# Kernel optimization log

Hardware: AMD Instinct MI355X
Metric: run time of the kernel (lower is better)

The kernel has to match this reference:

```python
import jax, jax.numpy as jnp
import numpy as np

VOCAB, EMBED, HIDDEN, NCLS, PAD = 50257, 512, 1024, 4, 0

def setup_inputs() -> dict:
    key = jax.random.key(0)
    k1, k2, k3, k4, k5, k6 = jax.random.split(key, 6)
    emb = jax.random.uniform(k1, (VOCAB, EMBED), jnp.float32, -0.1, 0.1)
    emb = emb.at[PAD].set(0.0)
    W = jax.random.normal(k2, (HIDDEN, EMBED), jnp.float32) * (2.0 / (EMBED + HIDDEN)) ** 0.5
    b_w = jnp.zeros((HIDDEN,), jnp.float32)
    U = jax.random.normal(k3, (HIDDEN, HIDDEN), jnp.float32) * (1.0 / HIDDEN) ** 0.5
    V = jax.random.normal(k4, (NCLS, HIDDEN), jnp.float32) * (2.0 / (HIDDEN + NCLS)) ** 0.5
    b_v = jnp.zeros((NCLS,), jnp.float32)
    x = jax.random.randint(k5, (64, 512), 0, VOCAB, jnp.int32)
    return {"x": x, "emb": emb, "W": W, "b_w": b_w, "U": U, "V": V, "b_v": b_v}

def reference(x, emb, W, b_w, U, V, b_v):
    # x: [B, S] int tokens. Dropouts are identity (eval mode).
    embedded = emb[x]                      # [B, S, E]
    # Precompute Wx for all timesteps in one GEMM: [B, S, H]
    wx = jnp.einsum('bse,he->bsh', embedded, W) + b_w
    B = x.shape[0]
    h0 = jnp.zeros((B, W.shape[0]), embedded.dtype)

    def step(h, wx_t):
        h = jnp.tanh(wx_t + h @ U.T)       # [B, H]
        return h, None

    h_final, _ = jax.lax.scan(step, h0, jnp.swapaxes(wx, 0, 1))  # scan over S
    return h_final @ V.T + b_v             # [B, NCLS]
```

## Files before the change

kernel.cpp:

```cpp
#include <hip/hip_runtime.h>
#include <stdint.h>

#define B 64
#define S 512
#define E 512
#define H 1024
#define NCLS 4

typedef __attribute__((ext_vector_type(8))) short short8;
typedef __attribute__((ext_vector_type(4))) float f32x4;

__device__ __forceinline__ unsigned short f32_to_bf16(float f) {
    unsigned int x = __float_as_uint(f);
    unsigned int r = (x + 0x7fffu + ((x >> 16) & 1u)) >> 16;
    return (unsigned short)r;
}
__device__ __forceinline__ float bf16_to_f32(unsigned short u) {
    return __uint_as_float(((unsigned int)u) << 16);
}

__device__ __forceinline__ void store_sc4u(unsigned int* p, unsigned int v) {
    asm volatile("global_store_dword %0, %1, off sc0 sc1"
                 :: "v"(p), "v"(v) : "memory");
}

#define K1_LDA 40

__global__ __launch_bounds__(256) void k_wx_gemm(
    const int* __restrict__ x, const float* __restrict__ emb,
    const float* __restrict__ W, const float* __restrict__ bw,
    unsigned short* __restrict__ wx)
{
    __shared__ unsigned short Asub[128 * K1_LDA];
    __shared__ unsigned short Bsub[128 * K1_LDA];

    const int t  = threadIdx.x;
    const int mt = blockIdx.x;
    const int nt = blockIdx.y;
    const int i0 = mt * 128;
    const int j0 = nt * 128;

    const int r  = t >> 1;
    const int kh = (t & 1) * 16;
    const int tok = x[i0 + r];
    const float* arow = emb + (size_t)tok * E;
    const float* brow = W + (size_t)(j0 + r) * E;

    const int lane = t & 63;
    const int w    = t >> 6;
    const int wm   = (w >> 1) * 64;
    const int wn   = (w & 1) * 64;
    const int fr   = lane & 15;
    const int kg   = lane >> 4;

    f32x4 acc[4][4] = {};

    for (int kt = 0; kt < E; kt += 32) {
        __syncthreads();
        {
            union { unsigned short us[8]; uint4 v; } p;
            const float* srcA = arow + kt + kh;
            #pragma unroll
            for (int i = 0; i < 8; ++i) p.us[i] = f32_to_bf16(srcA[i]);
            *(uint4*)&Asub[r * K1_LDA + kh] = p.v;
            #pragma unroll
            for (int i = 0; i < 8; ++i) p.us[i] = f32_to_bf16(srcA[8 + i]);
            *(uint4*)&Asub[r * K1_LDA + kh + 8] = p.v;
            const float* srcB = brow + kt + kh;
            #pragma unroll
            for (int i = 0; i < 8; ++i) p.us[i] = f32_to_bf16(srcB[i]);
            *(uint4*)&Bsub[r * K1_LDA + kh] = p.v;
            #pragma unroll
            for (int i = 0; i < 8; ++i) p.us[i] = f32_to_bf16(srcB[8 + i]);
            *(uint4*)&Bsub[r * K1_LDA + kh + 8] = p.v;
        }
        __syncthreads();

        short8 a[4], b[4];
        #pragma unroll
        for (int mi = 0; mi < 4; ++mi)
            a[mi] = *(const short8*)&Asub[(wm + mi * 16 + fr) * K1_LDA + kg * 8];
        #pragma unroll
        for (int ni = 0; ni < 4; ++ni)
            b[ni] = *(const short8*)&Bsub[(wn + ni * 16 + fr) * K1_LDA + kg * 8];
        #pragma unroll
        for (int mi = 0; mi < 4; ++mi)
            #pragma unroll
            for (int ni = 0; ni < 4; ++ni)
                acc[mi][ni] = __builtin_amdgcn_mfma_f32_16x16x32_bf16(
                                  a[mi], b[ni], acc[mi][ni], 0, 0, 0);
    }

    float bwv[4];
    #pragma unroll
    for (int ni = 0; ni < 4; ++ni) bwv[ni] = bw[j0 + wn + ni * 16 + fr];
    #pragma unroll
    for (int mi = 0; mi < 4; ++mi) {
        #pragma unroll
        for (int ni = 0; ni < 4; ++ni) {
            const int gn = j0 + wn + ni * 16 + fr;
            #pragma unroll
            for (int rr = 0; rr < 4; ++rr) {
                const int gm = i0 + wm + mi * 16 + kg * 4 + rr;
                const int bb = gm >> 9;
                const int ss = gm & 511;
                wx[(size_t)(ss * B + bb) * H + gn] =
                    f32_to_bf16(acc[mi][ni][rr] + bwv[ni]);
            }
        }
    }
}

__global__ __launch_bounds__(256) void k_rnn(
    const unsigned short* __restrict__ wx, const float* __restrict__ U,
    const float* __restrict__ Vw, const float* __restrict__ bv,
    unsigned int* __restrict__ hbuf, unsigned int* __restrict__ flags,
    float* __restrict__ out)
{
    __shared__ __align__(16) unsigned short Uhi[32 * 1024];
    __shared__ __align__(16) unsigned int Hh32[8 * 512];
    __shared__ __align__(16) unsigned int Hl32[8 * 512];
    __shared__ __align__(16) float redC[2][1024];

    const int t   = threadIdx.x;
    const int g   = blockIdx.x & 7;
    const int m   = blockIdx.x >> 3;
    const int j0  = m * 32;
    const int bg0 = g * 8;

    for (int rr = 0; rr < 32; ++rr) {
        f32x4 v = *(const f32x4*)(U + (size_t)(j0 + rr) * H + t * 4);
        uint2 hwd;
        hwd.x = f32_to_bf16(v[0]) | ((unsigned)f32_to_bf16(v[1]) << 16);
        hwd.y = f32_to_bf16(v[2]) | ((unsigned)f32_to_bf16(v[3]) << 16);
        const int byteoff = (rr * 2048 + t * 8) ^ ((rr & 7) << 4);
        *(uint2*)((char*)Uhi + byteoff) = hwd;
    }

    const int lane  = t & 63;
    const int w     = t >> 6;
    const int fr    = lane & 15;
    const int kg    = lane >> 4;
    const int kbase = w * 256;
    const int abrow = fr & 7;
    const int ob    = t >> 5;
    const int oj    = t & 31;

    unsigned int* fl = flags + g * 128;

    float wxv = bf16_to_f32(wx[(size_t)(bg0 + ob) * H + j0 + oj]);

    __syncthreads();

    for (int ts = 0; ts < S; ++ts) {
        const unsigned int* hr = hbuf + (ts & 1) * (B * H);
        unsigned int*       hw = hbuf + ((ts + 1) & 1) * (B * H);

        float wx_next = 0.f;
        if (ts + 1 < S)
            wx_next = bf16_to_f32(wx[(size_t)((ts + 1) * B + bg0 + ob) * H + j0 + oj]);

        {
            const unsigned int* fp = fl + w * 32 + (lane & 31);
            unsigned int fv;
            do {
                fv = __hip_atomic_load(fp, __ATOMIC_RELAXED,
                                       __HIP_MEMORY_SCOPE_AGENT);
            } while (!__all((int)(fv >= (unsigned)ts)));
        }

        {
            const unsigned long long* hb64 = (const unsigned long long*)hr;
            unsigned long long vv[16];
            #pragma unroll
            for (int i = 0; i < 16; ++i) {
                const int li = lane + 64 * i;
                const int b = li >> 7, col = li & 127;
                vv[i] = __hip_atomic_load(
                    hb64 + (size_t)(bg0 + b) * 512 + w * 128 + col,
                    __ATOMIC_RELAXED, __HIP_MEMORY_SCOPE_AGENT);
            }
            #pragma unroll
            for (int i = 0; i < 16; ++i) {
                const int li = lane + 64 * i;
                const int b = li >> 7;
                const int k2 = w * 128 + (li & 127);
                const unsigned int v0 = (unsigned int)vv[i];
                const unsigned int v1 = (unsigned int)(vv[i] >> 32);
                const int idx = (b * 512 + k2) ^ (b << 2);
                Hh32[idx] = (v0 >> 16) | (v1 & 0xffff0000u);
                Hl32[idx] = (v0 & 0xffffu) | (v1 << 16);
            }
        }

        f32x4 acc0 = {}, acc1 = {};
        #pragma unroll
        for (int kk = 0; kk < 8; ++kk) {
            const int k  = kbase + kk * 32 + kg * 8;
            const int ab = (abrow * 2048 + k * 2) ^ (abrow << 4);
            const short8 ahi = *(const short8*)((const char*)Hh32 + ab);
            const short8 alo = *(const short8*)((const char*)Hl32 + ab);
            const int b0 = (fr * 2048 + k * 2) ^ ((fr & 7) << 4);
            const int b1 = ((16 + fr) * 2048 + k * 2) ^ ((fr & 7) << 4);
            const short8 bh0 = *(const short8*)((const char*)Uhi + b0);
            const short8 bh1 = *(const short8*)((const char*)Uhi + b1);
            acc0 = __builtin_amdgcn_mfma_f32_16x16x32_bf16(ahi, bh0, acc0, 0, 0, 0);
            acc0 = __builtin_amdgcn_mfma_f32_16x16x32_bf16(alo, bh0, acc0, 0, 0, 0);
            acc1 = __builtin_amdgcn_mfma_f32_16x16x32_bf16(ahi, bh1, acc1, 0, 0, 0);
            acc1 = __builtin_amdgcn_mfma_f32_16x16x32_bf16(alo, bh1, acc1, 0, 0, 0);
        }

        float* rc = redC[ts & 1];
        if (kg < 2) {
            #pragma unroll
            for (int rr = 0; rr < 4; ++rr) {
                const int mb = kg * 4 + rr;
                rc[w * 256 + mb * 32 + fr]      = acc0[rr];
                rc[w * 256 + mb * 32 + 16 + fr] = acc1[rr];
            }
        }
        __syncthreads();

        float sum = rc[      ob * 32 + oj] + rc[256 + ob * 32 + oj]
                  + rc[512 + ob * 32 + oj] + rc[768 + ob * 32 + oj];

        float p = wxv + sum;
        p = fminf(fmaxf(p, -15.f), 15.f);
        const float e  = __expf(2.0f * p);
        const float hv = 1.0f - 2.0f / (e + 1.0f);

        const unsigned short hib = f32_to_bf16(hv);
        const unsigned short lob = f32_to_bf16(hv - bf16_to_f32(hib));
        store_sc4u(hw + (size_t)(bg0 + ob) * H + j0 + oj,
                   ((unsigned int)hib << 16) | lob);
        asm volatile("s_waitcnt vmcnt(0)" ::: "memory");
        if (lane == 0)
            __hip_atomic_store(&fl[m * 4 + w], (unsigned)(ts + 1),
                               __ATOMIC_RELAXED, __HIP_MEMORY_SCOPE_AGENT);
        wxv = wx_next;
    }

    if (m == 0) {
        if (t < 128)
            while (__hip_atomic_load(&fl[t], __ATOMIC_RELAXED,
                                     __HIP_MEMORY_SCOPE_AGENT) < (unsigned)S) {}
        __syncthreads();
        const unsigned int* hf = hbuf;
        const int o = t & 31, part = t >> 5;
        const int pb = o >> 2, c = o & 3;
        const unsigned long long* hrow =
            (const unsigned long long*)(hf + (size_t)(bg0 + pb) * H) + part * 64;
        const float* vrow = Vw + (size_t)c * H + part * 128;
        float partial = 0.f;
        for (int q = 0; q < 64; ++q) {
            unsigned long long vvq = __hip_atomic_load(hrow + q, __ATOMIC_RELAXED,
                                                       __HIP_MEMORY_SCOPE_AGENT);
            const unsigned int v0 = (unsigned int)vvq;
            const unsigned int v1 = (unsigned int)(vvq >> 32);
            const float h0 = bf16_to_f32((unsigned short)(v0 >> 16))
                           + bf16_to_f32((unsigned short)(v0 & 0xffffu));
            const float h1 = bf16_to_f32((unsigned short)(v1 >> 16))
                           + bf16_to_f32((unsigned short)(v1 & 0xffffu));
            partial += h0 * vrow[2 * q] + h1 * vrow[2 * q + 1];
        }
        __syncthreads();
        redC[0][part * 32 + o] = partial;
        __syncthreads();
        if (t < 32) {
            float sv = 0.f;
            #pragma unroll
            for (int pq = 0; pq < 8; ++pq) sv += redC[0][pq * 32 + t];
            out[(bg0 + (t >> 2)) * NCLS + (t & 3)] = sv + bv[t & 3];
        }
    }
}

extern "C" void kernel_launch(void* const* d_in, const int* in_sizes, int n_in,
                              void* d_out, int out_size, void* d_ws, size_t ws_size,
                              hipStream_t stream)
{
    const int*   x   = (const int*)d_in[0];
    const float* emb = (const float*)d_in[1];
    const float* W   = (const float*)d_in[2];
    const float* bw  = (const float*)d_in[3];
    const float* U   = (const float*)d_in[4];
    const float* V   = (const float*)d_in[5];
    const float* bv  = (const float*)d_in[6];
    float* out = (float*)d_out;

    unsigned short* wx = (unsigned short*)d_ws;
    const size_t WX_BYTES = (size_t)S * B * H * sizeof(unsigned short);
    unsigned int* hbuf = (unsigned int*)((char*)d_ws + WX_BYTES);
    const size_t HB_BYTES = (size_t)2 * B * H * sizeof(unsigned int);
    unsigned int* flags = (unsigned int*)((char*)d_ws + WX_BYTES + HB_BYTES);

    hipMemsetAsync((char*)d_ws + WX_BYTES, 0, HB_BYTES + 8192, stream);

    hipLaunchKernelGGL(k_wx_gemm, dim3(256, 8), dim3(256), 0, stream,
                       x, emb, W, bw, wx);
    hipLaunchKernelGGL(k_rnn, dim3(256), dim3(256), 0, stream,
                       wx, U, V, bv, hbuf, flags, out);
}
```

Before: 1.556 ms.

## Replace per-step block barrier with LDS counter and alternating publisher wave pairs

Removes the __syncthreads between the MFMA partial-sum stores and the tanh epilogue. Each wave now increments an LDS counter after writing its partials, and on alternating timesteps one pair of waves spins on that counter, does the reduction, applies tanh and publishes h and the flags. The other pair moves straight on to polling for the next step and prefetching wx. Flags are split into two parity banks of 64 entries each. This is meant to overlap the epilogue and global publish of one step with the flag wait and loads of the next, at the cost of more intricate memory ordering and LDS spin-waiting.

After: 3.585 ms. +130.4%, slower.

```diff
diff --git a/kernel.cpp b/kernel.cpp
--- a/kernel.cpp
+++ b/kernel.cpp
@@ -121,6 +121,7 @@
     __shared__ __align__(16) unsigned int Hh32[8 * 512];
     __shared__ __align__(16) unsigned int Hl32[8 * 512];
     __shared__ __align__(16) float redC[2][1024];
+    __shared__ unsigned int cnt[2];
 
     const int t   = threadIdx.x;
     const int g   = blockIdx.x & 7;
@@ -136,6 +137,7 @@
         const int byteoff = (rr * 2048 + t * 8) ^ ((rr & 7) << 4);
         *(uint2*)((char*)Uhi + byteoff) = hwd;
     }
+    if (t < 2) cnt[t] = 0u;
 
     const int lane  = t & 63;
     const int w     = t >> 6;
@@ -143,30 +145,41 @@
     const int kg    = lane >> 4;
     const int kbase = w * 256;
     const int abrow = fr & 7;
-    const int ob    = t >> 5;
-    const int oj    = t & 31;
+    const int pw    = w & 1;
+    const int o0  = pw * 128 + lane,  o1 = o0 + 64;
+    const int ob0 = o0 >> 5, oj0 = o0 & 31;
+    const int ob1 = o1 >> 5, oj1 = o1 & 31;
 
     unsigned int* fl = flags + g * 128;
 
-    float wxv = bf16_to_f32(wx[(size_t)(bg0 + ob) * H + j0 + oj]);
+    float wxv0 = 0.f, wxv1 = 0.f;
+    if ((w >> 1) == 0) {
+        wxv0 = bf16_to_f32(wx[(size_t)(bg0 + ob0) * H + j0 + oj0]);
+        wxv1 = bf16_to_f32(wx[(size_t)(bg0 + ob1) * H + j0 + oj1]);
+    }
 
     __syncthreads();
 
     for (int ts = 0; ts < S; ++ts) {
         const unsigned int* hr = hbuf + (ts & 1) * (B * H);
         unsigned int*       hw = hbuf + ((ts + 1) & 1) * (B * H);
-
-        float wx_next = 0.f;
-        if (ts + 1 < S)
-            wx_next = bf16_to_f32(wx[(size_t)((ts + 1) * B + bg0 + ob) * H + j0 + oj]);
+        const bool pub  = ((w >> 1) == (ts & 1));
+        const int  sin  = (ts + 1) & 1;
+        const int  spub = ts & 1;
 
         {
-            const unsigned int* fp = fl + w * 32 + (lane & 31);
+            const unsigned int* fp = fl + sin * 64 + 16 * w + (lane & 15);
             unsigned int fv;
             do {
                 fv = __hip_atomic_load(fp, __ATOMIC_RELAXED,
                                        __HIP_MEMORY_SCOPE_AGENT);
             } while (!__all((int)(fv >= (unsigned)ts)));
+        }
+
+        float wn0 = 0.f, wn1 = 0.f;
+        if (!pub && ts + 1 < S) {
+            wn0 = bf16_to_f32(wx[(size_t)((ts + 1) * B + bg0 + ob0) * H + j0 + oj0]);
+            wn1 = bf16_to_f32(wx[(size_t)((ts + 1) * B + bg0 + ob1) * H + j0 + oj1]);
         }
 
         {
@@ -210,7 +223,7 @@
             acc1 = __builtin_amdgcn_mfma_f32_16x16x32_bf16(alo, bh1, acc1, 0, 0, 0);
         }
 
-        float* rc = redC[ts & 1];
+        float* rc = redC[spub];
         if (kg < 2) {
             #pragma unroll
             for (int rr = 0; rr < 4; ++rr) {
@@ -219,30 +232,45 @@
                 rc[w * 256 + mb * 32 + 16 + fr] = acc1[rr];
             }
         }
-        __syncthreads();
-
-        float sum = rc[      ob * 32 + oj] + rc[256 + ob * 32 + oj]
-                  + rc[512 + ob * 32 + oj] + rc[768 + ob * 32 + oj];
-
-        float p = wxv + sum;
-        p = fminf(fmaxf(p, -15.f), 15.f);
-        const float e  = __expf(2.0f * p);
-        const float hv = 1.0f - 2.0f / (e + 1.0f);
-
-        const unsigned short hib = f32_to_bf16(hv);
-        const unsigned short lob = f32_to_bf16(hv - bf16_to_f32(hib));
-        store_sc4u(hw + (size_t)(bg0 + ob) * H + j0 + oj,
-                   ((unsigned int)hib << 16) | lob);
-        asm volatile("s_waitcnt vmcnt(0)" ::: "memory");
+        asm volatile("s_waitcnt lgkmcnt(0)" ::: "memory");
         if (lane == 0)
-            __hip_atomic_store(&fl[m * 4 + w], (unsigned)(ts + 1),
-                               __ATOMIC_RELAXED, __HIP_MEMORY_SCOPE_AGENT);
-        wxv = wx_next;
+            __hip_atomic_fetch_add(&cnt[spub], 1u, __ATOMIC_RELEASE,
+                                   __HIP_MEMORY_SCOPE_WORKGROUP);
+
+        if (pub) {
+            const unsigned int tgt = 4u * ((unsigned)(ts >> 1) + 1u);
+            while (__hip_atomic_load(&cnt[spub], __ATOMIC_ACQUIRE,
+                                     __HIP_MEMORY_SCOPE_WORKGROUP) < tgt) {}
+
+            float s0 = rc[o0] + rc[256 + o0] + rc[512 + o0] + rc[768 + o0];
+            float s1 = rc[o1] + rc[256 + o1] + rc[512 + o1] + rc[768 + o1];
+            float p0 = fminf(fmaxf(wxv0 + s0, -15.f), 15.f);
+            float p1 = fminf(fmaxf(wxv1 + s1, -15.f), 15.f);
+            const float e0 = __expf(2.0f * p0);
+            const float e1 = __expf(2.0f * p1);
+            const float h0 = 1.0f - 2.0f / (e0 + 1.0f);
+            const float h1 = 1.0f - 2.0f / (e1 + 1.0f);
+            const unsigned short h0b = f32_to_bf16(h0);
+            const unsigned short l0b = f32_to_bf16(h0 - bf16_to_f32(h0b));
+            const unsigned short h1b = f32_to_bf16(h1);
+            const unsigned short l1b = f32_to_bf16(h1 - bf16_to_f32(h1b));
+            store_sc4u(hw + (size_t)(bg0 + ob0) * H + j0 + oj0,
+                       ((unsigned int)h0b << 16) | l0b);
+            store_sc4u(hw + (size_t)(bg0 + ob1) * H + j0 + oj1,
+                       ((unsigned int)h1b << 16) | l1b);
+            asm volatile("s_waitcnt vmcnt(0)" ::: "memory");
+            if (lane == 0)
+                __hip_atomic_store(&fl[spub * 64 + m * 2 + pw],
+                                   (unsigned)(ts + 1), __ATOMIC_RELAXED,
+                                   __HIP_MEMORY_SCOPE_AGENT);
+        } else {
+            wxv0 = wn0; wxv1 = wn1;
+        }
     }
 
     if (m == 0) {
-        if (t < 128)
-            while (__hip_atomic_load(&fl[t], __ATOMIC_RELAXED,
+        if (t < 64)
+            while (__hip_atomic_load(&fl[64 + t], __ATOMIC_RELAXED,
                                      __HIP_MEMORY_SCOPE_AGENT) < (unsigned)S) {}
         __syncthreads();
         const unsigned int* hf = hbuf;
```
